# Performance work log

Hardware: AMD Instinct MI355X
Metric: run time of the kernel (lower is better)

Reference implementation:

```python
import jax, jax.numpy as jnp
import numpy as np

# Problem sizes (see shape_source)
C = 4096                      # sparse matrix is C x C
NUMEL = C * C                 # 16,777,216
S = 3355443                   # round(NUMEL * 0.2) sampled gradient entries
R = 1048576                   # result_quantity (top-k buffer size)
DECAY = 0.95                  # decay_constant
FRAC = S / float(NUMEL)       # fractional_sparsity (mask_active=False branch)


def setup_inputs() -> dict:
    key = jax.random.key(0)
    k1, k2, k3, k4 = jax.random.split(key, 4)
    # Sampled linear indices into the C x C grid (forward: torch.randint(0, numel, [S]))
    sample_index = jax.random.randint(k1, (S,), 0, NUMEL, dtype=jnp.int32)
    # Steady-state buffer of (row, col) pairs and their running gradient magnitudes
    result_index = jax.random.randint(k2, (R, 2), 0, C, dtype=jnp.int32)
    result_value = jax.random.uniform(k3, (R,), dtype=jnp.float32)
    # Incoming gradient on the sampled accumulator entries
    gradient = jax.random.normal(k4, (S,), dtype=jnp.float32)
    return {
        "sample_index": sample_index,
        "result_index": result_index,
        "result_value": result_value,
        "gradient": gradient,
    }


def reference(sample_index, result_index, result_value, gradient):
    """Faithful JAX version of StochasticSubSampler's backward-hook update:
    decay the stored buffer, take |gradient| on the new samples, coalesce
    duplicated (row, col) entries by summation, then keep the top-R values.
    Returns (new_result_index [R,2] int32, new_result_value [R] float32)."""
    adj_decay = 1.0 - FRAC * (1.0 - DECAY)  # adjusted decay constant

    # Linearized keys for coalescing. sample_index is already row*C + col.
    samp_keys = sample_index
    res_keys = result_index[:, 0] * C + result_index[:, 1]
    keys = jnp.concatenate([samp_keys, res_keys])               # [K]
    vals = jnp.concatenate([jnp.abs(gradient), adj_decay * result_value])  # [K]
    K = keys.shape[0]

    # Coalesce: sum values that share the same (row, col) key.
    uniq, inv = jnp.unique(keys, size=K, fill_value=-1, return_inverse=True)
    summed = jax.ops.segment_sum(vals, inv, num_segments=K)     # [K]
    counts = jax.ops.segment_sum(jnp.ones_like(vals), inv, num_segments=K)
    neg = jnp.finfo(jnp.float32).min
    summed = jnp.where(counts > 0, summed, neg)  # mask padded unique slots

    # Descending sort + top-R selection (argsort(-v)[:R] in the original).
    top_vals, top_pos = jax.lax.top_k(summed, R)
    top_keys = uniq[top_pos]
    new_index = jnp.stack([top_keys // C, top_keys % C], axis=-1)  # [R, 2]
    return new_index, top_vals
```

## Files before the change

### kernel.cpp

```cpp
#include <hip/hip_runtime.h>
#include <stdint.h>

#define CDIM   4096
#define S_N    3355443
#define R_N    1048576
#define N1     (S_N + R_N)
#define TILE   4096
#define WPT    (TILE / 256)
#define NTILES ((N1 + TILE - 1) / TILE)
#define NPAD   (NTILES * TILE)
#define NSB    (NPAD / 256)
#define SR_CH  ((NTILES + 255) / 256)
#define PAD_KEY 0xFFFFFFu
#define PAD_VAL 0xFFFFFFFFu
#define SENT  (((uint64_t)PAD_KEY << 32) | (uint64_t)PAD_VAL)
#define ADJF  ((float)(1.0 - (3355443.0 / 16777216.0) * (1.0 - 0.95)))

static __device__ __forceinline__ unsigned blockScanExcl(unsigned v, unsigned t,
                                                         unsigned* lw, unsigned* tot){
  unsigned lane = t & 63u, w = t >> 6;
  unsigned x = v;
  #pragma unroll
  for (int off = 1; off < 64; off <<= 1){
    unsigned y = __shfl_up(x, off, 64);
    if (lane >= (unsigned)off) x += y;
  }
  if (lane == 63u) lw[w] = x;
  __syncthreads();
  unsigned woff = 0;
  for (unsigned i = 0; i < w; i++) woff += lw[i];
  *tot = lw[0] + lw[1] + lw[2] + lw[3];
  __syncthreads();
  return x + woff - v;
}

static __device__ __forceinline__ uint64_t make_elem(unsigned i,
                                                     const int* __restrict__ sidx,
                                                     const int* __restrict__ ridx,
                                                     const float* __restrict__ rval,
                                                     const float* __restrict__ grad){
  uint32_t key, vb;
  if (i < S_N){
    key = (uint32_t)sidx[i];
    vb  = __float_as_uint(fabsf(grad[i]));
  } else if (i < N1){
    unsigned j = i - S_N;
    int2 rc = ((const int2* __restrict__)ridx)[j];
    key = (uint32_t)(rc.x * CDIM + rc.y);
    vb = __float_as_uint(ADJF * rval[j]);
  } else {
    key = PAD_KEY; vb = PAD_VAL;
  }
  return ((uint64_t)key << 32) | (uint64_t)vb;
}

__global__ __launch_bounds__(256) void k_hist0(const int* __restrict__ sidx,
                                               const int* __restrict__ ridx,
                                               unsigned* __restrict__ gh){
  __shared__ unsigned h[256];
  unsigned t = threadIdx.x;
  h[t] = 0; __syncthreads();
  size_t base = (size_t)blockIdx.x * TILE;
  #pragma unroll
  for (int r = 0; r < WPT; r++){
    unsigned i = (unsigned)(base + (size_t)r*256 + t);
    unsigned kb;
    if (i < S_N)       kb = ((uint32_t)sidx[i]) & 0xFFu;
    else if (i < N1)   kb = ((uint32_t)ridx[2u*(i - S_N) + 1u]) & 0xFFu;
    else               kb = 0xFFu;
    atomicAdd(&h[kb], 1u);
  }
  __syncthreads();
  gh[t * NTILES + blockIdx.x] = h[t];
}

__global__ __launch_bounds__(256) void k_hist(const uint64_t* __restrict__ in, unsigned shift,
                                              unsigned* __restrict__ gh){
  __shared__ unsigned h[256];
  unsigned t = threadIdx.x;
  h[t] = 0; __syncthreads();
  size_t base = (size_t)blockIdx.x * TILE;
  #pragma unroll
  for (int r = 0; r < WPT; r++){
    uint64_t e = in[base + (size_t)r*256 + t];
    atomicAdd(&h[(unsigned)((e >> shift) & 0xFF)], 1u);
  }
  __syncthreads();
  gh[t * NTILES + blockIdx.x] = h[t];
}

__global__ __launch_bounds__(256) void k_hist_syn(const uint64_t* __restrict__ in, unsigned shift,
                                                  unsigned* __restrict__ gh,
                                                  const unsigned* __restrict__ nsyn){
  __shared__ unsigned h[256];
  unsigned t = threadIdx.x;
  unsigned Un = nsyn[0];
  size_t base = (size_t)blockIdx.x * TILE;
  if (base >= (size_t)Un){
    gh[t * NTILES + blockIdx.x] = (t == 255u) ? (unsigned)TILE : 0u;
    return;
  }
  h[t] = 0; __syncthreads();
  #pragma unroll
  for (int r = 0; r < WPT; r++){
    unsigned i = (unsigned)(base + (size_t)r*256 + t);
    uint64_t e = (i < Un) ? in[i] : SENT;
    atomicAdd(&h[(unsigned)((e >> shift) & 0xFF)], 1u);
  }
  __syncthreads();
  gh[t * NTILES + blockIdx.x] = h[t];
}

__global__ __launch_bounds__(256) void k_scanrows(unsigned* __restrict__ gh,
                                                  unsigned* __restrict__ dtot){
  __shared__ unsigned lw[4];
  unsigned d = blockIdx.x, t = threadIdx.x;
  unsigned rowbase = d * NTILES;
  unsigned vals[SR_CH];
  unsigned s = 0;
  #pragma unroll
  for (int k = 0; k < SR_CH; k++){
    unsigned i = t * SR_CH + (unsigned)k;
    vals[k] = (i < NTILES) ? gh[rowbase + i] : 0u;
    s += vals[k];
  }
  unsigned tot;
  unsigned carry = blockScanExcl(s, t, lw, &tot);
  #pragma unroll
  for (int k = 0; k < SR_CH; k++){
    unsigned i = t * SR_CH + (unsigned)k;
    if (i < NTILES){ gh[rowbase + i] = carry; carry += vals[k]; }
  }
  if (t == 0) dtot[d] = tot;
}

template <int MODE>
__device__ __forceinline__ void scatter_body(const uint64_t* __restrict__ in,
                                             uint64_t* __restrict__ out,
                                             float* __restrict__ fout,
                                             unsigned shift,
                                             const unsigned* __restrict__ gh,
                                             const unsigned* __restrict__ dtot,
                                             const unsigned* __restrict__ nsyn,
                                             const unsigned* __restrict__ mskip,
                                             const int* __restrict__ sidx,
                                             const int* __restrict__ ridx,
                                             const float* __restrict__ rval,
                                             const float* __restrict__ grad,
                                             unsigned* __restrict__ mout){
  unsigned Un = 0u, M = 0u;
  if (MODE == 1 || MODE == 2 || MODE == 4){
    Un = nsyn[0];
    if (MODE != 4){
      M = mskip[0];
      if ((unsigned)blockIdx.x * TILE >= Un && M <= Un) return;
    }
  }
  __shared__ unsigned wrun[4*256];
  __shared__ unsigned gput[256];
  __shared__ unsigned lw[4];
  __shared__ unsigned cutm;
  __shared__ uint64_t stage[TILE];
  unsigned t = threadIdx.x, lane = t & 63u, w = t >> 6;
  wrun[t] = 0; wrun[256+t] = 0; wrun[512+t] = 0; wrun[768+t] = 0;
  __syncthreads();
  uint64_t ltm = (lane == 0) ? 0ull : (~0ull >> (64u - lane));
  uint64_t elems[WPT]; unsigned rnk[WPT]; unsigned dg[WPT];
  size_t base = (size_t)blockIdx.x * TILE + (size_t)w * (TILE/4);
  #pragma unroll
  for (int r = 0; r < WPT; r++){
    unsigned idx = (unsigned)(base + (size_t)r*64) + lane;
    uint64_t e;
    if (MODE == 3)      e = make_elem(idx, sidx, ridx, rval, grad);
    else if (MODE != 0) e = (idx < Un) ? in[idx] : SENT;
    else                e = in[idx];
    elems[r] = e;
    unsigned d = (unsigned)((e >> shift) & 0xFF);
    uint64_t m = ~0ull;
    #pragma unroll
    for (int b = 0; b < 8; b++){
      uint64_t bb = __ballot((d >> b) & 1u);
      m &= ((d >> b) & 1u) ? bb : ~bb;
    }
    unsigned rr   = (unsigned)__popcll(m & ltm);
    unsigned prev = wrun[w*256 + d];
    __builtin_amdgcn_wave_barrier();
    if (rr == 0) wrun[w*256 + d] = prev + (unsigned)__popcll(m);
    __builtin_amdgcn_wave_barrier();
    rnk[r] = prev + rr;
    dg[r]  = d;
  }
  __syncthreads();
  {
    unsigned d = t;
    unsigned c0 = wrun[d], c1 = wrun[256+d], c2 = wrun[512+d], c3 = wrun[768+d];
    unsigned cnt = c0 + c1 + c2 + c3;
    unsigned tot;
    unsigned ldig  = blockScanExcl(cnt, t, lw, &tot);
    unsigned tot2;
    unsigned dbase = blockScanExcl(dtot[d], t, lw, &tot2);
    if (MODE == 4){
      unsigned incl = dbase + dtot[d];
      if (dbase < R_N && incl >= R_N) cutm = incl;
    }
    gput[d] = dbase + gh[d * NTILES + blockIdx.x] - ldig;
    wrun[d]       = ldig;
    wrun[256 + d] = ldig + c0;
    wrun[512 + d] = ldig + c0 + c1;
    wrun[768 + d] = ldig + c0 + c1 + c2;
  }
  __syncthreads();
  if (MODE == 4){
    M = cutm;
    if (blockIdx.x == 0u && t == 0u) mout[0] = M;
  }
  #pragma unroll
  for (int r = 0; r < WPT; r++)
    stage[ wrun[w*256 + dg[r]] + rnk[r] ] = elems[r];
  __syncthreads();
  #pragma unroll
  for (int r = 0; r < WPT; r++){
    unsigned j = (unsigned)r * 256u + t;
    uint64_t e = stage[j];
    unsigned d = (unsigned)((e >> shift) & 0xFF);
    unsigned dest = gput[d] + j;
    if (MODE == 2){
      if (dest < R_N){
        uint32_t key = (uint32_t)(e >> 32);
        fout[2u*dest]        = (float)(key >> 12);
        fout[2u*dest + 1u]   = (float)(key & 4095u);
        fout[2u*R_N + dest]  = __uint_as_float(~(uint32_t)e);
      }
    } else if (MODE == 1 || MODE == 4){
      if (dest < M) out[dest] = e;
    } else {
      out[dest] = e;
    }
  }
}

__global__ __launch_bounds__(256) void k_scatter(const uint64_t* __restrict__ in,
                                                 uint64_t* __restrict__ out,
                                                 unsigned shift,
                                                 const unsigned* __restrict__ gh,
                                                 const unsigned* __restrict__ dtot){
  scatter_body<0>(in, out, nullptr, shift, gh, dtot, nullptr, nullptr,
                  nullptr, nullptr, nullptr, nullptr, nullptr);
}

__global__ __launch_bounds__(256) void k_scatter_b(const int* __restrict__ sidx,
                                                   const int* __restrict__ ridx,
                                                   const float* __restrict__ rval,
                                                   const float* __restrict__ grad,
                                                   uint64_t* __restrict__ out,
                                                   unsigned shift,
                                                   const unsigned* __restrict__ gh,
                                                   const unsigned* __restrict__ dtot){
  scatter_body<3>(nullptr, out, nullptr, shift, gh, dtot, nullptr, nullptr,
                  sidx, ridx, rval, grad, nullptr);
}

__global__ __launch_bounds__(256) void k_scatter_m(const uint64_t* __restrict__ in,
                                                   uint64_t* __restrict__ out,
                                                   unsigned shift,
                                                   const unsigned* __restrict__ gh,
                                                   const unsigned* __restrict__ dtot,
                                                   const unsigned* __restrict__ nsyn,
                                                   const unsigned* __restrict__ mskip){
  scatter_body<1>(in, out, nullptr, shift, gh, dtot, nsyn, mskip,
                  nullptr, nullptr, nullptr, nullptr, nullptr);
}

__global__ __launch_bounds__(256) void k_scatter_mc(const uint64_t* __restrict__ in,
                                                    uint64_t* __restrict__ out,
                                                    unsigned shift,
                                                    const unsigned* __restrict__ gh,
                                                    const unsigned* __restrict__ dtot,
                                                    const unsigned* __restrict__ nsyn,
                                                    unsigned* __restrict__ mout){
  scatter_body<4>(in, out, nullptr, shift, gh, dtot, nsyn, nullptr,
                  nullptr, nullptr, nullptr, nullptr, mout);
}

__global__ __launch_bounds__(256) void k_scatter_out(const uint64_t* __restrict__ in,
                                                     float* __restrict__ fout,
                                                     unsigned shift,
                                                     const unsigned* __restrict__ gh,
                                                     const unsigned* __restrict__ dtot,
                                                     const unsigned* __restrict__ nsyn){
  scatter_body<2>(in, nullptr, fout, shift, gh, dtot, nsyn, nsyn,
                  nullptr, nullptr, nullptr, nullptr, nullptr);
}

__global__ __launch_bounds__(256) void k_headcount(const uint64_t* __restrict__ in,
                                                   unsigned* __restrict__ hcnt){
  __shared__ unsigned wc[4];
  unsigned t = threadIdx.x, lane = t & 63u, w = t >> 6;
  size_t p = (size_t)blockIdx.x * 256 + t;
  uint64_t e = in[p];
  uint32_t k = (uint32_t)(e >> 32);
  bool head = ((p == 0) || ((uint32_t)(in[p-1] >> 32) != k)) && ((uint32_t)e != PAD_VAL);
  uint64_t m = __ballot(head);
  if (lane == 0) wc[w] = (unsigned)__popcll(m);
  __syncthreads();
  if (t == 0) hcnt[blockIdx.x] = wc[0] + wc[1] + wc[2] + wc[3];
}

__global__ __launch_bounds__(256) void k_scanheads(unsigned* __restrict__ hcnt,
                                                   unsigned* __restrict__ utot){
  __shared__ unsigned short buf[NSB];
  __shared__ unsigned lw[4];
  unsigned t = threadIdx.x;
  for (unsigned i = t; i < NSB; i += 256) buf[i] = (unsigned short)hcnt[i];
  __syncthreads();
  const unsigned CH = (NSB + 255) / 256;
  unsigned s = 0;
  for (unsigned k = 0; k < CH; k++){
    unsigned i = t * CH + k;
    if (i < NSB) s += buf[i];
  }
  unsigned tot;
  unsigned carry = blockScanExcl(s, t, lw, &tot);
  for (unsigned k = 0; k < CH; k++){
    unsigned i = t * CH + k;
    if (i < NSB){ unsigned v = buf[i]; hcnt[i] = carry; carry += v; }
  }
  if (t == 0) utot[0] = tot;
}

__global__ __launch_bounds__(256) void k_segsum(const uint64_t* __restrict__ in,
                                                uint64_t* __restrict__ out,
                                                const unsigned* __restrict__ hbase){
  __shared__ unsigned wc[4], woffs[4];
  unsigned t = threadIdx.x, lane = t & 63u, w = t >> 6;
  size_t p = (size_t)blockIdx.x * 256 + t;
  uint64_t e0 = in[p];
  uint32_t k = (uint32_t)(e0 >> 32);
  bool head = ((p == 0) || ((uint32_t)(in[p-1] >> 32) != k)) && ((uint32_t)e0 != PAD_VAL);
  uint64_t m = __ballot(head);
  if (lane == 0) wc[w] = (unsigned)__popcll(m);
  __syncthreads();
  if (t == 0){ unsigned a = 0; for (int i = 0; i < 4; i++){ woffs[i] = a; a += wc[i]; } }
  __syncthreads();
  if (head){
    uint64_t ltm = (lane == 0) ? 0ull : (~0ull >> (64u - lane));
    unsigned rank = (unsigned)__popcll(m & ltm);
    unsigned oidx = hbase[blockIdx.x] + woffs[w] + rank;
    float s = __uint_as_float((uint32_t)e0);
    size_t q = p + 1;
    while (q < NPAD){
      uint64_t e = in[q];
      if ((uint32_t)(e >> 32) != k) break;
      uint32_t vb = (uint32_t)e;
      if (vb == PAD_VAL) break;
      s += __uint_as_float(vb);
      q++;
    }
    out[oidx] = ((uint64_t)k << 32) | (uint64_t)(uint32_t)(~__float_as_uint(s));
  }
}

extern "C" void kernel_launch(void* const* d_in, const int* in_sizes, int n_in,
                              void* d_out, int out_size, void* d_ws, size_t ws_size,
                              hipStream_t stream) {
  const int*   sidx = (const int*)d_in[0];
  const int*   ridx = (const int*)d_in[1];
  const float* rval = (const float*)d_in[2];
  const float* grad = (const float*)d_in[3];
  float* out = (float*)d_out;

  uint64_t* A0   = (uint64_t*)d_ws;
  uint64_t* A1   = A0 + NPAD;
  unsigned* gh   = (unsigned*)(A1 + NPAD);
  unsigned* dtot = gh + 256 * NTILES;
  unsigned* hcnt = dtot + 256;
  unsigned* utot = hcnt + NSB;
  unsigned* mvar = utot + 1;

  k_hist0    <<<NTILES, 256, 0, stream>>>(sidx, ridx, gh);
  k_scanrows <<<256,    256, 0, stream>>>(gh, dtot);
  k_scatter_b<<<NTILES, 256, 0, stream>>>(sidx, ridx, rval, grad, A1, 32, gh, dtot);
  k_hist     <<<NTILES, 256, 0, stream>>>(A1, 40, gh);
  k_scanrows <<<256,    256, 0, stream>>>(gh, dtot);
  k_scatter  <<<NTILES, 256, 0, stream>>>(A1, A0, 40, gh, dtot);
  k_hist     <<<NTILES, 256, 0, stream>>>(A0, 48, gh);
  k_scanrows <<<256,    256, 0, stream>>>(gh, dtot);
  k_scatter  <<<NTILES, 256, 0, stream>>>(A0, A1, 48, gh, dtot);

  k_headcount<<<NSB, 256, 0, stream>>>(A1, hcnt);
  k_scanheads<<<1,   256, 0, stream>>>(hcnt, utot);
  k_segsum   <<<NSB, 256, 0, stream>>>(A1, A0, hcnt);

  k_hist_syn  <<<NTILES, 256, 0, stream>>>(A0, 24, gh, utot);
  k_scanrows  <<<256,    256, 0, stream>>>(gh, dtot);
  k_scatter_mc<<<NTILES, 256, 0, stream>>>(A0, A1, 24, gh, dtot, utot, mvar);

  k_hist_syn <<<NTILES, 256, 0, stream>>>(A1, 0, gh, mvar);
  k_scanrows <<<256,    256, 0, stream>>>(gh, dtot);
  k_scatter_m<<<NTILES, 256, 0, stream>>>(A1, A0, 0, gh, dtot, mvar, mvar);
  k_hist_syn <<<NTILES, 256, 0, stream>>>(A0, 8, gh, mvar);
  k_scanrows <<<256,    256, 0, stream>>>(gh, dtot);
  k_scatter_m<<<NTILES, 256, 0, stream>>>(A0, A1, 8, gh, dtot, mvar, mvar);
  k_hist_syn <<<NTILES, 256, 0, stream>>>(A1, 16, gh, mvar);
  k_scanrows <<<256,    256, 0, stream>>>(gh, dtot);
  k_scatter_m<<<NTILES, 256, 0, stream>>>(A1, A0, 16, gh, dtot, mvar, mvar);
  k_hist_syn   <<<NTILES, 256, 0, stream>>>(A0, 24, gh, mvar);
  k_scanrows   <<<256,    256, 0, stream>>>(gh, dtot);
  k_scatter_out<<<NTILES, 256, 0, stream>>>(A0, out, 24, gh, dtot, mvar);
}
```

Before: 412.1 us.

## Fuse head count, scan and segment sum into single-pass look-back kernel

Replaces the separate head-count, single-block scan and segmented-sum kernels with one kernel that computes per-block head counts and obtains its output offset via decoupled look-back over atomic flags. Look-back flags are zeroed inside the first histogram kernel. This removes two launches and an extra full pass over the sorted pair array. In exchange it relies on forward-progress of earlier blocks and adds spin-waiting on global atomics.

```diff
diff --git a/kernel.cpp b/kernel.cpp
--- a/kernel.cpp
+++ b/kernel.cpp
@@ -56,11 +56,14 @@
 
 __global__ __launch_bounds__(256) void k_hist0(const int* __restrict__ sidx,
                                                const int* __restrict__ ridx,
-                                               unsigned* __restrict__ gh){
+                                               unsigned* __restrict__ gh,
+                                               unsigned* __restrict__ lb){
   __shared__ unsigned h[256];
-  unsigned t = threadIdx.x;
-  h[t] = 0; __syncthreads();
-  size_t base = (size_t)blockIdx.x * TILE;
+  unsigned t = threadIdx.x, b = blockIdx.x;
+  h[t] = 0;
+  if (t < 16u) lb[b * 16u + t] = 0u;
+  __syncthreads();
+  size_t base = (size_t)b * TILE;
   #pragma unroll
   for (int r = 0; r < WPT; r++){
     unsigned i = (unsigned)(base + (size_t)r*256 + t);
@@ -71,7 +74,7 @@
     atomicAdd(&h[kb], 1u);
   }
   __syncthreads();
-  gh[t * NTILES + blockIdx.x] = h[t];
+  gh[t * NTILES + b] = h[t];
 }
 
 __global__ __launch_bounds__(256) void k_hist(const uint64_t* __restrict__ in, unsigned shift,
@@ -292,48 +295,14 @@
                   nullptr, nullptr, nullptr, nullptr, nullptr);
 }
 
-__global__ __launch_bounds__(256) void k_headcount(const uint64_t* __restrict__ in,
-                                                   unsigned* __restrict__ hcnt){
-  __shared__ unsigned wc[4];
-  unsigned t = threadIdx.x, lane = t & 63u, w = t >> 6;
-  size_t p = (size_t)blockIdx.x * 256 + t;
-  uint64_t e = in[p];
-  uint32_t k = (uint32_t)(e >> 32);
-  bool head = ((p == 0) || ((uint32_t)(in[p-1] >> 32) != k)) && ((uint32_t)e != PAD_VAL);
-  uint64_t m = __ballot(head);
-  if (lane == 0) wc[w] = (unsigned)__popcll(m);
-  __syncthreads();
-  if (t == 0) hcnt[blockIdx.x] = wc[0] + wc[1] + wc[2] + wc[3];
-}
-
-__global__ __launch_bounds__(256) void k_scanheads(unsigned* __restrict__ hcnt,
-                                                   unsigned* __restrict__ utot){
-  __shared__ unsigned short buf[NSB];
-  __shared__ unsigned lw[4];
-  unsigned t = threadIdx.x;
-  for (unsigned i = t; i < NSB; i += 256) buf[i] = (unsigned short)hcnt[i];
-  __syncthreads();
-  const unsigned CH = (NSB + 255) / 256;
-  unsigned s = 0;
-  for (unsigned k = 0; k < CH; k++){
-    unsigned i = t * CH + k;
-    if (i < NSB) s += buf[i];
-  }
-  unsigned tot;
-  unsigned carry = blockScanExcl(s, t, lw, &tot);
-  for (unsigned k = 0; k < CH; k++){
-    unsigned i = t * CH + k;
-    if (i < NSB){ unsigned v = buf[i]; hcnt[i] = carry; carry += v; }
-  }
-  if (t == 0) utot[0] = tot;
-}
-
-__global__ __launch_bounds__(256) void k_segsum(const uint64_t* __restrict__ in,
-                                                uint64_t* __restrict__ out,
-                                                const unsigned* __restrict__ hbase){
+__global__ __launch_bounds__(256) void k_coalesce(const uint64_t* __restrict__ in,
+                                                  uint64_t* __restrict__ out,
+                                                  unsigned* __restrict__ lb,
+                                                  unsigned* __restrict__ utot){
   __shared__ unsigned wc[4], woffs[4];
-  unsigned t = threadIdx.x, lane = t & 63u, w = t >> 6;
-  size_t p = (size_t)blockIdx.x * 256 + t;
+  __shared__ unsigned hb;
+  unsigned b = blockIdx.x, t = threadIdx.x, lane = t & 63u, w = t >> 6;
+  size_t p = (size_t)b * 256 + t;
   uint64_t e0 = in[p];
   uint32_t k = (uint32_t)(e0 >> 32);
   bool head = ((p == 0) || ((uint32_t)(in[p-1] >> 32) != k)) && ((uint32_t)e0 != PAD_VAL);
@@ -341,11 +310,51 @@
   if (lane == 0) wc[w] = (unsigned)__popcll(m);
   __syncthreads();
   if (t == 0){ unsigned a = 0; for (int i = 0; i < 4; i++){ woffs[i] = a; a += wc[i]; } }
+  if (w == 0u){
+    unsigned cnt = wc[0] + wc[1] + wc[2] + wc[3];
+    if (lane == 0u)
+      __hip_atomic_store(&lb[b], ((b == 0u) ? (2u<<30) : (1u<<30)) | cnt,
+                         __ATOMIC_RELEASE, __HIP_MEMORY_SCOPE_AGENT);
+    unsigned run = 0u;
+    if (b > 0u){
+      int p0 = (int)b - 1;
+      for (;;){
+        int idx = p0 - (int)lane;
+        unsigned v2 = (idx >= 0)
+          ? __hip_atomic_load(&lb[idx], __ATOMIC_ACQUIRE, __HIP_MEMORY_SCOPE_AGENT)
+          : (2u << 30);
+        if (__ballot((v2 >> 30) == 0u)){ __builtin_amdgcn_s_sleep(1); continue; }
+        unsigned long long im = __ballot((v2 >> 30) == 2u);
+        unsigned cv = v2 & 0x3FFFFFFFu;
+        bool fin = (im != 0ull);
+        unsigned contrib;
+        if (fin){
+          unsigned li = (unsigned)__ffsll((long long)im) - 1u;
+          contrib = (lane <= li) ? cv : 0u;
+        } else {
+          contrib = cv;
+        }
+        #pragma unroll
+        for (int off = 1; off < 64; off <<= 1)
+          contrib += (unsigned)__shfl_xor((int)contrib, off, 64);
+        run += contrib;
+        if (fin) break;
+        p0 -= 64;
+      }
+      if (lane == 0u)
+        __hip_atomic_store(&lb[b], (2u<<30) | (run + cnt),
+                           __ATOMIC_RELEASE, __HIP_MEMORY_SCOPE_AGENT);
+    }
+    if (lane == 0u){
+      hb = run;
+      if (b == (unsigned)(NSB - 1)) utot[0] = run + cnt;
+    }
+  }
   __syncthreads();
   if (head){
     uint64_t ltm = (lane == 0) ? 0ull : (~0ull >> (64u - lane));
     unsigned rank = (unsigned)__popcll(m & ltm);
-    unsigned oidx = hbase[blockIdx.x] + woffs[w] + rank;
+    unsigned oidx = hb + woffs[w] + rank;
     float s = __uint_as_float((uint32_t)e0);
     size_t q = p + 1;
     while (q < NPAD){
@@ -373,11 +382,11 @@
   uint64_t* A1   = A0 + NPAD;
   unsigned* gh   = (unsigned*)(A1 + NPAD);
   unsigned* dtot = gh + 256 * NTILES;
-  unsigned* hcnt = dtot + 256;
-  unsigned* utot = hcnt + NSB;
+  unsigned* lb   = dtot + 256;
+  unsigned* utot = lb + NSB;
   unsigned* mvar = utot + 1;
 
-  k_hist0    <<<NTILES, 256, 0, stream>>>(sidx, ridx, gh);
+  k_hist0    <<<NTILES, 256, 0, stream>>>(sidx, ridx, gh, lb);
   k_scanrows <<<256,    256, 0, stream>>>(gh, dtot);
   k_scatter_b<<<NTILES, 256, 0, stream>>>(sidx, ridx, rval, grad, A1, 32, gh, dtot);
   k_hist     <<<NTILES, 256, 0, stream>>>(A1, 40, gh);
@@ -387,9 +396,7 @@
   k_scanrows <<<256,    256, 0, stream>>>(gh, dtot);
   k_scatter  <<<NTILES, 256, 0, stream>>>(A0, A1, 48, gh, dtot);
 
-  k_headcount<<<NSB, 256, 0, stream>>>(A1, hcnt);
-  k_scanheads<<<1,   256, 0, stream>>>(hcnt, utot);
-  k_segsum   <<<NSB, 256, 0, stream>>>(A1, A0, hcnt);
+  k_coalesce<<<NSB, 256, 0, stream>>>(A1, A0, lb, utot);
 
   k_hist_syn  <<<NTILES, 256, 0, stream>>>(A0, 24, gh, utot);
   k_scanrows  <<<256,    256, 0, stream>>>(gh, dtot);
```

After: 1.605 ms. 3.89x slower.

## Replace compacted segment-sum with gapped per-block output, removing headcount and scan kernels

Applied to the files above, without the earlier changes.

The separate head-count and head-scan kernels are removed. The segment-sum kernel now writes unique entries at a fixed per-256 block offset, leaving gaps, and records each block's head count. The next radix histogram and scatter read those per-block counts and substitute sentinels for the empty slots, so compaction happens inside the following sort pass. This drops two launches and one full read pass over the sorted array. In exchange, the first post-coalesce histogram and scatter must process every tile, since the early exit on the unique count is gone, and they do an extra count lookup per element.

```diff
diff --git a/kernel.cpp b/kernel.cpp
--- a/kernel.cpp
+++ b/kernel.cpp
@@ -58,9 +58,9 @@
                                                const int* __restrict__ ridx,
                                                unsigned* __restrict__ gh){
   __shared__ unsigned h[256];
-  unsigned t = threadIdx.x;
+  unsigned t = threadIdx.x, b = blockIdx.x;
   h[t] = 0; __syncthreads();
-  size_t base = (size_t)blockIdx.x * TILE;
+  size_t base = (size_t)b * TILE;
   #pragma unroll
   for (int r = 0; r < WPT; r++){
     unsigned i = (unsigned)(base + (size_t)r*256 + t);
@@ -71,7 +71,7 @@
     atomicAdd(&h[kb], 1u);
   }
   __syncthreads();
-  gh[t * NTILES + blockIdx.x] = h[t];
+  gh[t * NTILES + b] = h[t];
 }
 
 __global__ __launch_bounds__(256) void k_hist(const uint64_t* __restrict__ in, unsigned shift,
@@ -109,6 +109,23 @@
   }
   __syncthreads();
   gh[t * NTILES + blockIdx.x] = h[t];
+}
+
+__global__ __launch_bounds__(256) void k_hist_syn2(const uint64_t* __restrict__ in, unsigned shift,
+                                                   unsigned* __restrict__ gh,
+                                                   const unsigned* __restrict__ hcnt){
+  __shared__ unsigned h[256];
+  unsigned t = threadIdx.x, b = blockIdx.x;
+  h[t] = 0; __syncthreads();
+  size_t base = (size_t)b * TILE;
+  #pragma unroll
+  for (int r = 0; r < WPT; r++){
+    unsigned cnt = hcnt[b * 16u + (unsigned)r];
+    uint64_t e = (t < cnt) ? in[base + (size_t)r*256 + t] : SENT;
+    atomicAdd(&h[(unsigned)((e >> shift) & 0xFF)], 1u);
+  }
+  __syncthreads();
+  gh[t * NTILES + b] = h[t];
 }
 
 __global__ __launch_bounds__(256) void k_scanrows(unsigned* __restrict__ gh,
@@ -147,14 +164,13 @@
                                              const int* __restrict__ ridx,
                                              const float* __restrict__ rval,
                                              const float* __restrict__ grad,
+                                             const unsigned* __restrict__ hcnt,
                                              unsigned* __restrict__ mout){
   unsigned Un = 0u, M = 0u;
-  if (MODE == 1 || MODE == 2 || MODE == 4){
+  if (MODE == 1 || MODE == 2){
     Un = nsyn[0];
-    if (MODE != 4){
-      M = mskip[0];
-      if ((unsigned)blockIdx.x * TILE >= Un && M <= Un) return;
-    }
+    M = mskip[0];
+    if ((unsigned)blockIdx.x * TILE >= Un && M <= Un) return;
   }
   __shared__ unsigned wrun[4*256];
   __shared__ unsigned gput[256];
@@ -171,9 +187,17 @@
   for (int r = 0; r < WPT; r++){
     unsigned idx = (unsigned)(base + (size_t)r*64) + lane;
     uint64_t e;
-    if (MODE == 3)      e = make_elem(idx, sidx, ridx, rval, grad);
-    else if (MODE != 0) e = (idx < Un) ? in[idx] : SENT;
-    else                e = in[idx];
+    if (MODE == 3){
+      e = make_elem(idx, sidx, ridx, rval, grad);
+    } else if (MODE == 4){
+      unsigned cnt = hcnt[blockIdx.x * 16u + (w << 2) + ((unsigned)r >> 2)];
+      unsigned sl  = (((unsigned)r & 3u) << 6) + lane;
+      e = (sl < cnt) ? in[idx] : SENT;
+    } else if (MODE != 0){
+      e = (idx < Un) ? in[idx] : SENT;
+    } else {
+      e = in[idx];
+    }
     elems[r] = e;
     unsigned d = (unsigned)((e >> shift) & 0xFF);
     uint64_t m = ~0ull;
@@ -245,7 +269,7 @@
                                                  const unsigned* __restrict__ gh,
                                                  const unsigned* __restrict__ dtot){
   scatter_body<0>(in, out, nullptr, shift, gh, dtot, nullptr, nullptr,
-                  nullptr, nullptr, nullptr, nullptr, nullptr);
+                  nullptr, nullptr, nullptr, nullptr, nullptr, nullptr);
 }
 
 __global__ __launch_bounds__(256) void k_scatter_b(const int* __restrict__ sidx,
@@ -257,7 +281,7 @@
                                                    const unsigned* __restrict__ gh,
                                                    const unsigned* __restrict__ dtot){
   scatter_body<3>(nullptr, out, nullptr, shift, gh, dtot, nullptr, nullptr,
-                  sidx, ridx, rval, grad, nullptr);
+                  sidx, ridx, rval, grad, nullptr, nullptr);
 }
 
 __global__ __launch_bounds__(256) void k_scatter_m(const uint64_t* __restrict__ in,
@@ -268,18 +292,18 @@
                                                    const unsigned* __restrict__ nsyn,
                                                    const unsigned* __restrict__ mskip){
   scatter_body<1>(in, out, nullptr, shift, gh, dtot, nsyn, mskip,
-                  nullptr, nullptr, nullptr, nullptr, nullptr);
-}
-
-__global__ __launch_bounds__(256) void k_scatter_mc(const uint64_t* __restrict__ in,
+                  nullptr, nullptr, nullptr, nullptr, nullptr, nullptr);
+}
+
+__global__ __launch_bounds__(256) void k_scatter_mg(const uint64_t* __restrict__ in,
                                                     uint64_t* __restrict__ out,
                                                     unsigned shift,
                                                     const unsigned* __restrict__ gh,
                                                     const unsigned* __restrict__ dtot,
-                                                    const unsigned* __restrict__ nsyn,
+                                                    const unsigned* __restrict__ hcnt,
                                                     unsigned* __restrict__ mout){
-  scatter_body<4>(in, out, nullptr, shift, gh, dtot, nsyn, nullptr,
-                  nullptr, nullptr, nullptr, nullptr, mout);
+  scatter_body<4>(in, out, nullptr, shift, gh, dtot, nullptr, nullptr,
+                  nullptr, nullptr, nullptr, nullptr, hcnt, mout);
 }
 
 __global__ __launch_bounds__(256) void k_scatter_out(const uint64_t* __restrict__ in,
@@ -289,48 +313,12 @@
                                                      const unsigned* __restrict__ dtot,
                                                      const unsigned* __restrict__ nsyn){
   scatter_body<2>(in, nullptr, fout, shift, gh, dtot, nsyn, nsyn,
-                  nullptr, nullptr, nullptr, nullptr, nullptr);
-}
-
-__global__ __launch_bounds__(256) void k_headcount(const uint64_t* __restrict__ in,
-                                                   unsigned* __restrict__ hcnt){
-  __shared__ unsigned wc[4];
-  unsigned t = threadIdx.x, lane = t & 63u, w = t >> 6;
-  size_t p = (size_t)blockIdx.x * 256 + t;
-  uint64_t e = in[p];
-  uint32_t k = (uint32_t)(e >> 32);
-  bool head = ((p == 0) || ((uint32_t)(in[p-1] >> 32) != k)) && ((uint32_t)e != PAD_VAL);
-  uint64_t m = __ballot(head);
-  if (lane == 0) wc[w] = (unsigned)__popcll(m);
-  __syncthreads();
-  if (t == 0) hcnt[blockIdx.x] = wc[0] + wc[1] + wc[2] + wc[3];
-}
-
-__global__ __launch_bounds__(256) void k_scanheads(unsigned* __restrict__ hcnt,
-                                                   unsigned* __restrict__ utot){
-  __shared__ unsigned short buf[NSB];
-  __shared__ unsigned lw[4];
-  unsigned t = threadIdx.x;
-  for (unsigned i = t; i < NSB; i += 256) buf[i] = (unsigned short)hcnt[i];
-  __syncthreads();
-  const unsigned CH = (NSB + 255) / 256;
-  unsigned s = 0;
-  for (unsigned k = 0; k < CH; k++){
-    unsigned i = t * CH + k;
-    if (i < NSB) s += buf[i];
-  }
-  unsigned tot;
-  unsigned carry = blockScanExcl(s, t, lw, &tot);
-  for (unsigned k = 0; k < CH; k++){
-    unsigned i = t * CH + k;
-    if (i < NSB){ unsigned v = buf[i]; hcnt[i] = carry; carry += v; }
-  }
-  if (t == 0) utot[0] = tot;
-}
-
-__global__ __launch_bounds__(256) void k_segsum(const uint64_t* __restrict__ in,
-                                                uint64_t* __restrict__ out,
-                                                const unsigned* __restrict__ hbase){
+                  nullptr, nullptr, nullptr, nullptr, nullptr, nullptr);
+}
+
+__global__ __launch_bounds__(256) void k_segsum2(const uint64_t* __restrict__ in,
+                                                 uint64_t* __restrict__ out,
+                                                 unsigned* __restrict__ hcnt){
   __shared__ unsigned wc[4], woffs[4];
   unsigned t = threadIdx.x, lane = t & 63u, w = t >> 6;
   size_t p = (size_t)blockIdx.x * 256 + t;
@@ -340,12 +328,16 @@
   uint64_t m = __ballot(head);
   if (lane == 0) wc[w] = (unsigned)__popcll(m);
   __syncthreads();
-  if (t == 0){ unsigned a = 0; for (int i = 0; i < 4; i++){ woffs[i] = a; a += wc[i]; } }
+  if (t == 0){
+    unsigned a = 0;
+    for (int i = 0; i < 4; i++){ woffs[i] = a; a += wc[i]; }
+    hcnt[blockIdx.x] = a;
+  }
   __syncthreads();
   if (head){
     uint64_t ltm = (lane == 0) ? 0ull : (~0ull >> (64u - lane));
     unsigned rank = (unsigned)__popcll(m & ltm);
-    unsigned oidx = hbase[blockIdx.x] + woffs[w] + rank;
+    unsigned oidx = blockIdx.x * 256u + woffs[w] + rank;
     float s = __uint_as_float((uint32_t)e0);
     size_t q = p + 1;
     while (q < NPAD){
@@ -374,8 +366,7 @@
   unsigned* gh   = (unsigned*)(A1 + NPAD);
   unsigned* dtot = gh + 256 * NTILES;
   unsigned* hcnt = dtot + 256;
-  unsigned* utot = hcnt + NSB;
-  unsigned* mvar = utot + 1;
+  unsigned* mvar = hcnt + NSB;
 
   k_hist0    <<<NTILES, 256, 0, stream>>>(sidx, ridx, gh);
   k_scanrows <<<256,    256, 0, stream>>>(gh, dtot);
@@ -387,13 +378,11 @@
   k_scanrows <<<256,    256, 0, stream>>>(gh, dtot);
   k_scatter  <<<NTILES, 256, 0, stream>>>(A0, A1, 48, gh, dtot);
 
-  k_headcount<<<NSB, 256, 0, stream>>>(A1, hcnt);
-  k_scanheads<<<1,   256, 0, stream>>>(hcnt, utot);
-  k_segsum   <<<NSB, 256, 0, stream>>>(A1, A0, hcnt);
-
-  k_hist_syn  <<<NTILES, 256, 0, stream>>>(A0, 24, gh, utot);
-  k_scanrows  <<<256,    256, 0, stream>>>(gh, dtot);
-  k_scatter_mc<<<NTILES, 256, 0, stream>>>(A0, A1, 24, gh, dtot, utot, mvar);
+  k_segsum2<<<NSB, 256, 0, stream>>>(A1, A0, hcnt);
+
+  k_hist_syn2<<<NTILES, 256, 0, stream>>>(A0, 24, gh, hcnt);
+  k_scanrows <<<256,    256, 0, stream>>>(gh, dtot);
+  k_scatter_mg<<<NTILES, 256, 0, stream>>>(A0, A1, 24, gh, dtot, hcnt, mvar);
 
   k_hist_syn <<<NTILES, 256, 0, stream>>>(A1, 0, gh, mvar);
   k_scanrows <<<256,    256, 0, stream>>>(gh, dtot);
```

After: 389.5 us (median of 2 runs). 1.06x faster.
